# Kernel optimization log

Hardware: AMD Instinct MI355X
Metric: run time of the kernel (lower is better)

The kernel has to match this reference:

```python
import jax, jax.numpy as jnp
import numpy as np

DEPTH, C, HS, NH, WS, B = 10, 128, 512, 8, 2, 4096


def _sincos_1d(embed_dim, pos):
    omega = np.arange(embed_dim // 2, dtype=np.float64)
    omega /= embed_dim / 2.0
    omega = 1.0 / 10000 ** omega
    out = np.einsum('m,d->md', pos.reshape(-1), omega)
    return np.concatenate([np.sin(out), np.cos(out)], axis=1)


def _sincos_pos_embed(embed_dim, grid_size):
    g = np.arange(grid_size, dtype=np.float32)
    grid = np.stack(np.meshgrid(g, g), axis=0).reshape(2, -1)
    emb_h = _sincos_1d(embed_dim // 2, grid[0])
    emb_w = _sincos_1d(embed_dim // 2, grid[1])
    return np.concatenate([emb_h, emb_w], axis=1)  # (16, HS)


def _encode_board(x):
    # x: (B,128) int piece ids -> (B,12,8,8) one-hot planes (vectorized encodeBoard)
    x = x.reshape(-1, 2, 8, 8)
    pieces = jnp.arange(1, 7)
    white = (x[:, 0, None, :, :] == pieces[None, :, None, None]).astype(jnp.float32)
    black = (x[:, 1, None, :, :] == pieces[None, :, None, None]).astype(jnp.float32)
    return jnp.concatenate([white, black], axis=1)


def _conv3x3(x, w, b):
    y = jax.lax.conv_general_dilated(x, w, (1, 1), 'SAME',
                                     dimension_numbers=('NCHW', 'OIHW', 'NCHW'))
    return y + b[None, :, None, None]


def _bn(x, g, b, eps=1e-5):
    # training-mode BatchNorm2d: per-batch stats over (N,H,W)
    m = x.mean((0, 2, 3), keepdims=True)
    v = x.var((0, 2, 3), keepdims=True)
    return (x - m) * jax.lax.rsqrt(v + eps) * g[None, :, None, None] + b[None, :, None, None]


def _ln(x, eps=1e-6):
    m = x.mean(-1, keepdims=True)
    v = x.var(-1, keepdims=True)
    return (x - m) * jax.lax.rsqrt(v + eps)


def _window_partition(x, ws):
    b, c, h, w = x.shape
    x = x.reshape(b, c, h // ws, ws, w // ws, ws)
    x = x.transpose(0, 2, 4, 3, 5, 1)  # b h w p1 p2 c
    return x.reshape(b, (h // ws) * (w // ws), ws * ws * c)


def _window_reverse(win, ws, h, w):
    b, n, d = win.shape
    c = d // (ws * ws)
    x = win.reshape(b, h // ws, w // ws, ws, ws, c)
    x = x.transpose(0, 5, 1, 3, 2, 4)  # b c h p1 w p2
    return x.reshape(b, c, h, w)


def _attention(t, qkv_w, qkv_b, proj_w, proj_b):
    b, n, d = t.shape
    hd = d // NH
    qkv = (t @ qkv_w + qkv_b).reshape(b, n, 3, NH, hd)
    q, k, v = jnp.moveaxis(qkv, 2, 0)  # each (b,n,NH,hd)
    attn = jax.nn.softmax(jnp.einsum('bqhd,bkhd->bhqk', q * hd ** -0.5, k), axis=-1)
    out = jnp.einsum('bhqk,bkhd->bqhd', attn, v).reshape(b, n, d)
    return out @ proj_w + proj_b


def _block(x, pos, p):
    (rb1_w, rb1_b, g1, b1, rb2_w, rb2_b, g2, b2,
     qkv_w, qkv_b, proj_w, proj_b, f1_w, f1_b, f2_w, f2_b) = p
    h, w = x.shape[2], x.shape[3]
    z = _bn(_conv3x3(jax.nn.relu(x), rb1_w, rb1_b), g1, b1)
    z = _bn(_conv3x3(jax.nn.relu(z), rb2_w, rb2_b), g2, b2)
    x = x + z
    t = _window_partition(x, WS) + pos
    t = t + _ln(_attention(t, qkv_w, qkv_b, proj_w, proj_b))
    t = t + _ln(jax.nn.relu(t @ f1_w + f1_b) @ f2_w + f2_b)
    return _window_reverse(t, WS, h, w)


def _forward(x, pos_embed, conv1_w, conv1_b, blk, lin1_w, lin1_b, lin2_w, lin2_b):
    h = _conv3x3(_encode_board(x), conv1_w, conv1_b)

    def step(h, p):
        return _block(h, pos_embed, p), None

    h, _ = jax.lax.scan(step, h, blk)
    feat = h.transpose(0, 2, 3, 1).reshape(h.shape[0], -1)  # B (H W C)
    logits = jax.nn.relu(feat @ lin1_w + lin1_b) @ lin2_w + lin2_b
    return jax.nn.softmax(logits, axis=1)


def setup_inputs() -> dict:
    key = jax.random.key(0)
    ks = jax.random.split(key, 16)
    n = lambda k, shp: jax.random.normal(k, shp, dtype=jnp.float32) * 0.02
    inp = {}
    inp['x'] = jax.random.randint(ks[0], (B, 128), 0, 7)
    inp['pos_embed'] = jnp.asarray(_sincos_pos_embed(HS, 8 // WS), dtype=jnp.float32)[None]
    inp['conv1_w'] = n(ks[1], (C, 12, 3, 3))
    inp['conv1_b'] = jnp.zeros((C,), jnp.float32)
    inp['rb1_w'] = n(ks[2], (DEPTH, C, C, 3, 3)); inp['rb1_b'] = jnp.zeros((DEPTH, C), jnp.float32)
    inp['bn1_g'] = jnp.ones((DEPTH, C), jnp.float32); inp['bn1_b'] = jnp.zeros((DEPTH, C), jnp.float32)
    inp['rb2_w'] = n(ks[3], (DEPTH, C, C, 3, 3)); inp['rb2_b'] = jnp.zeros((DEPTH, C), jnp.float32)
    inp['bn2_g'] = jnp.ones((DEPTH, C), jnp.float32); inp['bn2_b'] = jnp.zeros((DEPTH, C), jnp.float32)
    inp['qkv_w'] = n(ks[4], (DEPTH, HS, 3 * HS)); inp['qkv_b'] = jnp.zeros((DEPTH, 3 * HS), jnp.float32)
    inp['proj_w'] = n(ks[5], (DEPTH, HS, HS)); inp['proj_b'] = jnp.zeros((DEPTH, HS), jnp.float32)
    inp['fc1_w'] = n(ks[6], (DEPTH, HS, HS)); inp['fc1_b'] = jnp.zeros((DEPTH, HS), jnp.float32)
    inp['fc2_w'] = n(ks[7], (DEPTH, HS, HS)); inp['fc2_b'] = jnp.zeros((DEPTH, HS), jnp.float32)
    inp['lin1_w'] = n(ks[8], (C * 64, 1024)); inp['lin1_b'] = jnp.zeros((1024,), jnp.float32)
    inp['lin2_w'] = n(ks[9], (1024, 640)); inp['lin2_b'] = jnp.zeros((640,), jnp.float32)
    return inp


def reference(x, pos_embed, conv1_w, conv1_b, rb1_w, rb1_b, bn1_g, bn1_b,
              rb2_w, rb2_b, bn2_g, bn2_b, qkv_w, qkv_b, proj_w, proj_b,
              fc1_w, fc1_b, fc2_w, fc2_b, lin1_w, lin1_b, lin2_w, lin2_b):
    blk = (rb1_w, rb1_b, bn1_g, bn1_b, rb2_w, rb2_b, bn2_g, bn2_b,
           qkv_w, qkv_b, proj_w, proj_b, fc1_w, fc1_b, fc2_w, fc2_b)
    return _forward(x, pos_embed, conv1_w, conv1_b, blk, lin1_w, lin1_b, lin2_w, lin2_b)
```

## Files before the change

### kernel.cpp

```cpp
#include <hip/hip_runtime.h>
#include <hip/hip_fp16.h>
#include <math.h>


#define NBATCH 4096
#define NPOSR  (NBATCH*64)
#define CH     1024
#define CHT    (CH*16)

#define OFF_ACT   0
#define OFF_BIG2  33554432
#define OFF_WT1   (OFF_BIG2 + 16777216)
#define OFF_WTA   (OFF_WT1 + 13824)
#define OFF_WTB   (OFF_WTA + 737280)
#define OFF_WTT   (OFF_WTB + 737280)
#define OFF_STATS (OFF_WTT + 786432)
#define OFF_BNP   (OFF_STATS + 256)
#define OFF_BIAS  (OFF_BNP + 256)
#define WS_NEED_FLOATS (OFF_BIAS + 1536)

#define H_QKVB 0
#define H_ATT  25165824
#define H_PRJ  0
#define H_T2H  8388608
#define H_LOG  8388608

#define T_QKV  0
#define T_PRJ  786432
#define T_F1   1048576
#define T_F2   1310720

typedef _Float16 f16x8 __attribute__((ext_vector_type(8)));
typedef _Float16 f16x4 __attribute__((ext_vector_type(4)));
typedef float f32x4 __attribute__((ext_vector_type(4)));

__device__ inline f32x4 vzero4() { f32x4 z; z[0]=0.f; z[1]=0.f; z[2]=0.f; z[3]=0.f; return z; }

__device__ inline float4 ld_half4(const __half* p) {
  float2 a = __half22float2(*(const __half2*)p);
  float2 b = __half22float2(*(const __half2*)(p + 2));
  return make_float4(a.x, a.y, b.x, b.y);
}

__device__ __forceinline__ void gll16(const void* g, void* lds) {
  __builtin_amdgcn_global_load_lds(
      (__attribute__((address_space(1))) void*)g,
      (__attribute__((address_space(3))) void*)lds,
      16, 0, 0);
}

__global__ void k_zero(float* __restrict__ s) { s[threadIdx.x] = 0.f; }

__global__ void k_sentinel(float* __restrict__ out, int n, float val) {
  for (int i = blockIdx.x*blockDim.x + threadIdx.x; i < n; i += gridDim.x*blockDim.x)
    out[i] = val;
}

__global__ void k_wprep(const float* __restrict__ src, float* __restrict__ dst, int L, int Cin) {
  int total = L * 128 * Cin * 9;
  for (int idx = blockIdx.x*blockDim.x + threadIdx.x; idx < total; idx += gridDim.x*blockDim.x) {
    int kk = idx % 9; int t2 = idx / 9;
    int ci = t2 % Cin; t2 /= Cin;
    int co = t2 % 128; int l  = t2 / 128;
    dst[((size_t)(l*9 + kk)*Cin + ci)*128 + co] = src[idx];
  }
}

__global__ void k_wprep16(const float* __restrict__ src, __half* __restrict__ dst, int L) {
  int total = L * 128 * 128 * 9;
  for (int idx = blockIdx.x*blockDim.x + threadIdx.x; idx < total; idx += gridDim.x*blockDim.x) {
    int kk = idx % 9; int t2 = idx / 9;
    int ci = t2 % 128; t2 /= 128;
    int co = t2 % 128; int l  = t2 / 128;
    dst[((size_t)(l*128 + co))*1152 + kk*128 + ci] = __float2half(src[idx]);
  }
}

__global__ void k_wt16(const float* __restrict__ W, __half* __restrict__ WT, int K, int N) {
  int total = K * N;
  for (int idx = blockIdx.x*blockDim.x + threadIdx.x; idx < total; idx += gridDim.x*blockDim.x) {
    int k = idx / N, n = idx % N;
    WT[(size_t)n*K + k] = __float2half(W[idx]);
  }
}

__global__ void k_wt16x4(const float* __restrict__ Wq, const float* __restrict__ Wp,
                         const float* __restrict__ W1, const float* __restrict__ W2,
                         const float* __restrict__ bq,
                         __half* __restrict__ wTt, float* __restrict__ biasbuf) {
  int gid0 = blockIdx.x*blockDim.x + threadIdx.x;
  if (gid0 < 1536) biasbuf[gid0] = bq[gid0] * (gid0 < 512 ? 0.125f : 1.f);
  const int TOT = 786432 + 3*262144;
  for (int idx = gid0; idx < TOT; idx += gridDim.x*blockDim.x) {
    if (idx < 786432) {
      int k = idx / 1536, n = idx % 1536;
      float v = Wq[idx] * (n < 512 ? 0.125f : 1.f);
      wTt[T_QKV + (size_t)n*512 + k] = __float2half(v);
    } else {
      int r0 = idx - 786432;
      int s = r0 / 262144, r = r0 % 262144;
      int k = r / 512, n = r % 512;
      const float* W = (s == 0) ? Wp : (s == 1) ? W1 : W2;
      wTt[T_PRJ + s*262144 + (size_t)n*512 + k] = __float2half(W[r]);
    }
  }
}

__global__ __launch_bounds__(256) void k_conv1(const int* __restrict__ xin,
    const float* __restrict__ wT1, const float* __restrict__ b1,
    float* __restrict__ out) {
  __shared__ int s_w[64], s_b[64];
  int b = blockIdx.x, t = threadIdx.x;
  if (t < 64) { s_w[t] = xin[b*128 + t]; s_b[t] = xin[b*128 + 64 + t]; }
  __syncthreads();
  int p = t >> 2, i = t & 3;
  int y = p >> 3, x = p & 7;
  float acc[32];
  #pragma unroll
  for (int j = 0; j < 32; ++j) acc[j] = b1[i*32 + j];
  #pragma unroll
  for (int kk = 0; kk < 9; ++kk) {
    int ny = y + kk/3 - 1, nx = x + kk%3 - 1;
    if (ny < 0 || ny > 7 || nx < 0 || nx > 7) continue;
    int np = ny*8 + nx;
    int wp = s_w[np], bp = s_b[np];
    if (wp >= 1 && wp <= 6) {
      const float* w = &wT1[(size_t)(kk*12 + (wp-1))*128 + i*32];
      #pragma unroll
      for (int j = 0; j < 32; ++j) acc[j] += w[j];
    }
    if (bp >= 1 && bp <= 6) {
      const float* w = &wT1[(size_t)(kk*12 + 6 + (bp-1))*128 + i*32];
      #pragma unroll
      for (int j = 0; j < 32; ++j) acc[j] += w[j];
    }
  }
  float* o = &out[((size_t)b*64 + p)*128 + i*32];
  #pragma unroll
  for (int j = 0; j < 8; ++j)
    *(float4*)&o[j*4] = make_float4(acc[j*4], acc[j*4+1], acc[j*4+2], acc[j*4+3]);
}

__device__ inline float cvt_in(float v) { return v; }
__device__ inline float cvt_in(__half v) { return __half2float(v); }

#define IMG_W 136

template<typename TIN>
__global__ __launch_bounds__(256) void k_conv_mfma(const TIN* __restrict__ in,
    const __half* __restrict__ wT , const float* __restrict__ bias,
    const float* __restrict__ bnp, int use_bn, __half* __restrict__ out,
    float* __restrict__ stats) {
  __shared__ __align__(16) _Float16 s_img[2*65*IMG_W];
  __shared__ __align__(16) _Float16 s_B[2][4096];
  __shared__ float s_sum[128], s_sq[128];
  int b2 = blockIdx.x, t = threadIdx.x;
  int w = t >> 6, lane = t & 63;

  auto issueB = [&](int win, int buf) {
    #pragma unroll
    for (int i = 0; i < 2; ++i) {
      int rbase = (w*2 + i)*16;
      const __half* g = &wT[(size_t)(rbase + (lane>>2))*1152 + win*32 + (lane&3)*8];
      gll16(g, &s_B[buf][rbase*32]);
    }
  };
  issueB(0, 0);

  for (int idx4 = t; idx4 < 4096; idx4 += 256) {
    int img = idx4 >> 11, rr = (idx4 >> 5) & 63, c4 = (idx4 & 31) * 4;
    const TIN* src = &in[((size_t)(b2*2 + img)*64 + rr)*128 + c4];
    float v0 = cvt_in(src[0]), v1 = cvt_in(src[1]), v2 = cvt_in(src[2]), v3 = cvt_in(src[3]);
    if (use_bn) {
      v0 = bnp[c4+0]*v0 + bnp[128+c4+0];
      v1 = bnp[c4+1]*v1 + bnp[128+c4+1];
      v2 = bnp[c4+2]*v2 + bnp[128+c4+2];
      v3 = bnp[c4+3]*v3 + bnp[128+c4+3];
    }
    f16x4 h;
    h[0] = (_Float16)fmaxf(v0, 0.f); h[1] = (_Float16)fmaxf(v1, 0.f);
    h[2] = (_Float16)fmaxf(v2, 0.f); h[3] = (_Float16)fmaxf(v3, 0.f);
    *(f16x4*)&s_img[(img*65 + rr)*IMG_W + c4] = h;
  }
  {
    int img = t >> 7, c = t & 127;
    s_img[(img*65 + 64)*IMG_W + c] = (_Float16)0.f;
    if (t < 128) { s_sum[t] = 0.f; s_sq[t] = 0.f; }
  }
  int wm = (w >> 1)*64, wn = (w & 1)*64;
  int fr = lane & 15, fq = lane >> 4;
  int imgo[4], yy[4], xx_[4];
  #pragma unroll
  for (int mt = 0; mt < 4; ++mt) {
    int r = wm + mt*16 + fr;
    imgo[mt] = r >> 6; int p = r & 63; yy[mt] = p >> 3; xx_[mt] = p & 7;
  }
  f32x4 acc[4][4];
  #pragma unroll
  for (int mt = 0; mt < 4; ++mt)
    #pragma unroll
    for (int nt = 0; nt < 4; ++nt) acc[mt][nt] = vzero4();
  __syncthreads();

  #pragma unroll
  for (int kk = 0; kk < 9; ++kk) {
    int dy = kk/3 - 1, dx = kk%3 - 1;
    const _Float16* abase[4];
    #pragma unroll
    for (int mt = 0; mt < 4; ++mt) {
      int ny = yy[mt] + dy, nx = xx_[mt] + dx;
      int row = ((unsigned)ny < 8u && (unsigned)nx < 8u) ? (ny*8 + nx) : 64;
      abase[mt] = &s_img[(imgo[mt]*65 + row)*IMG_W];
    }
    #pragma unroll
    for (int q = 0; q < 4; ++q) {
      int win = kk*4 + q;
      int buf = win & 1;
      if (win + 1 < 36) issueB(win + 1, buf ^ 1);
      f16x8 af[4], bf[4];
      #pragma unroll
      for (int mt = 0; mt < 4; ++mt) af[mt] = *(const f16x8*)&abase[mt][q*32 + fq*8];
      #pragma unroll
      for (int nt = 0; nt < 4; ++nt) bf[nt] = *(const f16x8*)&s_B[buf][(wn + nt*16 + fr)*32 + fq*8];
      #pragma unroll
      for (int mt = 0; mt < 4; ++mt)
        #pragma unroll
        for (int nt = 0; nt < 4; ++nt)
          acc[mt][nt] = __builtin_amdgcn_mfma_f32_16x16x32_f16(af[mt], bf[nt], acc[mt][nt], 0, 0, 0);
      __syncthreads();
    }
  }
  #pragma unroll
  for (int nt = 0; nt < 4; ++nt) {
    int col = wn + nt*16 + fr;
    float bv = bias[col];
    float s = 0.f, q = 0.f;
    #pragma unroll
    for (int mt = 0; mt < 4; ++mt) {
      int rbase = wm + mt*16 + fq*4;
      #pragma unroll
      for (int j = 0; j < 4; ++j) {
        int r = rbase + j;
        int img = r >> 6, p = r & 63;
        float v = acc[mt][nt][j] + bv;
        s += v; q += v*v;
        out[((size_t)(b2*2 + img)*64 + p)*128 + col] = __float2half(v);
      }
    }
    s += __shfl_xor(s, 16); s += __shfl_xor(s, 32);
    q += __shfl_xor(q, 16); q += __shfl_xor(q, 32);
    if (fq == 0) { atomicAdd(&s_sum[col], s); atomicAdd(&s_sq[col], q); }
  }
  __syncthreads();
  if (t < 128) {
    atomicAdd(&stats[t], s_sum[t]);
    atomicAdd(&stats[128 + t], s_sq[t]);
  }
}

__global__ void k_bnfin(float* __restrict__ stats, const float* __restrict__ g,
                        const float* __restrict__ bb, float* __restrict__ bnp) {
  int c = threadIdx.x;
  const float invN = 1.f / (float)NPOSR;
  float m = stats[c] * invN;
  float v = stats[128+c] * invN - m*m;
  float sc = g[c] * rsqrtf(v + 1e-5f);
  bnp[c] = sc;
  bnp[128+c] = bb[c] - m*sc;
  stats[c] = 0.f; stats[128+c] = 0.f;
}

__global__ __launch_bounds__(256) void k_make_t(float* __restrict__ act,
    const __half* __restrict__ z1h, const float* __restrict__ bnp,
    const float* __restrict__ pos) {
  __shared__ float s_t[8192];
  int b = blockIdx.x, t = threadIdx.x;
  for (int idx4 = t; idx4 < 2048; idx4 += 256) {
    int n = idx4 >> 7, d4 = idx4 & 127;
    int d = d4*4, c = d & 127, q = d >> 7;
    int y = ((n>>2)<<1) + (q>>1), xx = ((n&3)<<1) + (q&1);
    size_t sp = ((size_t)b*64 + y*8 + xx)*128 + c;
    float4 a  = *(const float4*)&act[sp];
    float4 z  = ld_half4(&z1h[sp]);
    float4 sc = *(const float4*)&bnp[c];
    float4 sh = *(const float4*)&bnp[128+c];
    float4 pe = *(const float4*)&pos[n*512 + d];
    float4 o;
    o.x = a.x + sc.x*z.x + sh.x + pe.x;
    o.y = a.y + sc.y*z.y + sh.y + pe.y;
    o.z = a.z + sc.z*z.z + sh.z + pe.z;
    o.w = a.w + sc.w*z.w + sh.w + pe.w;
    *(float4*)&s_t[n*512 + d] = o;
  }
  __syncthreads();
  for (int idx4 = t; idx4 < 2048; idx4 += 256)
    *(float4*)&act[(size_t)b*8192 + idx4*4] = *(float4*)&s_t[idx4*4];
}

#define QS 1544

__global__ __launch_bounds__(256) void k_attn16(const __half* __restrict__ qkvbuf,
    __half* __restrict__ attnout) {
  __shared__ __align__(16) _Float16 s_qkv[16][QS];
  __shared__ float S[8][16][17];
  int img = blockIdx.x, t = threadIdx.x;
  const __half* src = qkvbuf + (size_t)img*16*1536;
  #pragma unroll
  for (int i = 0; i < 12; ++i) {
    int lin = t + i*256;
    int row = lin / 192, c8 = lin % 192;
    *(f16x8*)&s_qkv[row][c8*8] = *(const f16x8*)&src[(size_t)row*1536 + c8*8];
  }
  __syncthreads();
  {
    int h = t >> 5, qi = (t >> 1) & 15, ko = (t & 1) * 8;
    int rot = t & 31;
    float acc[8];
    #pragma unroll
    for (int k = 0; k < 8; ++k) acc[k] = 0.f;
    const __half2* qr = (const __half2*)&s_qkv[qi][h*64];
    for (int i2 = 0; i2 < 32; ++i2) {
      int d2 = (i2 + rot) & 31;
      float2 q2 = __half22float2(qr[d2]);
      #pragma unroll
      for (int k = 0; k < 8; ++k) {
        float2 k2 = __half22float2(*(const __half2*)&s_qkv[ko + k][512 + h*64 + d2*2]);
        acc[k] += q2.x*k2.x + q2.y*k2.y;
      }
    }
    #pragma unroll
    for (int k = 0; k < 8; ++k) S[h][qi][ko + k] = acc[k];
  }
  __syncthreads();
  if (t < 128) {
    int h = t >> 4, qi = t & 15;
    float* Sr = S[h][qi];
    float mx = -1e30f;
    #pragma unroll
    for (int ki = 0; ki < 16; ++ki) mx = fmaxf(mx, Sr[ki]);
    float sm = 0.f; float e[16];
    #pragma unroll
    for (int ki = 0; ki < 16; ++ki) { e[ki] = expf(Sr[ki] - mx); sm += e[ki]; }
    float inv = 1.f / sm;
    #pragma unroll
    for (int ki = 0; ki < 16; ++ki) Sr[ki] = e[ki]*inv;
  }
  __syncthreads();
  {
    int qi = t >> 4, rem = t & 15;
    int h = rem >> 1, dhb = (rem & 1) * 32;
    int rot = (t >> 2) & 15;
    float P[16];
    #pragma unroll
    for (int k = 0; k < 16; ++k) P[k] = S[h][qi][(k + rot) & 15];
    __half* orow = attnout + ((size_t)img*16 + qi)*512 + h*64 + dhb;
    #pragma unroll
    for (int j = 0; j < 16; ++j) {
      int dh = dhb + 2*j;
      float a0 = 0.f, a1 = 0.f;
      #pragma unroll
      for (int kk2 = 0; kk2 < 16; ++kk2) {
        int ki = (kk2 + rot) & 15;
        float2 v2 = __half22float2(*(const __half2*)&s_qkv[ki][1024 + h*64 + dh]);
        a0 += P[kk2]*v2.x; a1 += P[kk2]*v2.y;
      }
      *(__half2*)&orow[2*j] = __floats2half2_rn(a0, a1);
    }
  }
}

template<int MTI, int A16, int B16, int RELU, int OUT16>
__global__ __launch_bounds__(256) void k_mgemm(const void* __restrict__ Ap,
    const void* __restrict__ Bp, const float* __restrict__ bias,
    void* __restrict__ Cp, int M, int N, int K) {
  constexpr int BM = MTI*32;
  __shared__ __align__(16) _Float16 sA[2][BM*32];
  __shared__ __align__(16) _Float16 sB[2][128*32];
  int t = threadIdx.x;
  int bm = blockIdx.x * BM, bn = blockIdx.y * 128;
  int w = t >> 6, lane = t & 63;
  int wm = (w >> 1) * (MTI*16), wn = (w & 1) * 64;
  int fr = lane & 15, fq = lane >> 4;

  auto stageA = [&](int k0, int buf) {
    if (A16) {
      const __half* A = (const __half*)Ap;
      constexpr int NI = MTI/2;
      #pragma unroll
      for (int i = 0; i < NI; ++i) {
        int rbase = (w*NI + i)*16;
        gll16(&A[(size_t)(bm + rbase + (lane>>2))*K + k0 + (lane&3)*8],
              &sA[buf][rbase*32]);
      }
    } else {
      const float* A = (const float*)Ap;
      if (MTI == 4) {
        int srow = t >> 1, skh = (t & 1) * 16;
        const float4* src = (const float4*)&A[(size_t)(bm + srow)*K + k0 + skh];
        float4 v0 = src[0], v1 = src[1], v2 = src[2], v3 = src[3];
        f16x8 h0, h1;
        h0[0]=(_Float16)v0.x; h0[1]=(_Float16)v0.y; h0[2]=(_Float16)v0.z; h0[3]=(_Float16)v0.w;
        h0[4]=(_Float16)v1.x; h0[5]=(_Float16)v1.y; h0[6]=(_Float16)v1.z; h0[7]=(_Float16)v1.w;
        h1[0]=(_Float16)v2.x; h1[1]=(_Float16)v2.y; h1[2]=(_Float16)v2.z; h1[3]=(_Float16)v2.w;
        h1[4]=(_Float16)v3.x; h1[5]=(_Float16)v3.y; h1[6]=(_Float16)v3.z; h1[7]=(_Float16)v3.w;
        *(f16x8*)&sA[buf][srow*32 + skh]     = h0;
        *(f16x8*)&sA[buf][srow*32 + skh + 8] = h1;
      } else {
        int srow = t >> 2, g8 = (t & 3) * 8;
        const float4* src = (const float4*)&A[(size_t)(bm + srow)*K + k0 + g8];
        float4 v0 = src[0], v1 = src[1];
        f16x8 h0;
        h0[0]=(_Float16)v0.x; h0[1]=(_Float16)v0.y; h0[2]=(_Float16)v0.z; h0[3]=(_Float16)v0.w;
        h0[4]=(_Float16)v1.x; h0[5]=(_Float16)v1.y; h0[6]=(_Float16)v1.z; h0[7]=(_Float16)v1.w;
        *(f16x8*)&sA[buf][srow*32 + g8] = h0;
      }
    }
  };
  auto stageB = [&](int k0, int buf) {
    if (B16) {
      const __half* BT = (const __half*)Bp;
      #pragma unroll
      for (int i = 0; i < 2; ++i) {
        int rbase = (w*2 + i)*16;
        gll16(&BT[(size_t)(bn + rbase + (lane>>2))*K + k0 + (lane&3)*8],
              &sB[buf][rbase*32]);
      }
    } else {
      const float* B = (const float*)Bp;
      int kr = t >> 3, n0 = (t & 7) * 16;
      #pragma unroll
      for (int g = 0; g < 4; ++g) {
        float4 v = *(const float4*)&B[(size_t)(k0 + kr)*N + bn + n0 + g*4];
        sB[buf][(n0+g*4+0)*32 + kr] = (_Float16)v.x;
        sB[buf][(n0+g*4+1)*32 + kr] = (_Float16)v.y;
        sB[buf][(n0+g*4+2)*32 + kr] = (_Float16)v.z;
        sB[buf][(n0+g*4+3)*32 + kr] = (_Float16)v.w;
      }
    }
  };

  f32x4 acc[MTI][4];
  #pragma unroll
  for (int mt = 0; mt < MTI; ++mt)
    #pragma unroll
    for (int nt = 0; nt < 4; ++nt) acc[mt][nt] = vzero4();

  stageA(0, 0); stageB(0, 0);
  __syncthreads();
  int KW = K >> 5;
  for (int kw = 0; kw < KW; ++kw) {
    int buf = kw & 1;
    if (kw + 1 < KW) { stageA((kw+1)*32, buf ^ 1); stageB((kw+1)*32, buf ^ 1); }
    f16x8 af[MTI], bf[4];
    #pragma unroll
    for (int mt = 0; mt < MTI; ++mt) af[mt] = *(const f16x8*)&sA[buf][(wm + mt*16 + fr)*32 + fq*8];
    #pragma unroll
    for (int nt = 0; nt < 4; ++nt) bf[nt] = *(const f16x8*)&sB[buf][(wn + nt*16 + fr)*32 + fq*8];
    #pragma unroll
    for (int mt = 0; mt < MTI; ++mt)
      #pragma unroll
      for (int nt = 0; nt < 4; ++nt)
        acc[mt][nt] = __builtin_amdgcn_mfma_f32_16x16x32_f16(af[mt], bf[nt], acc[mt][nt], 0, 0, 0);
    __syncthreads();
  }
  #pragma unroll
  for (int mt = 0; mt < MTI; ++mt)
    #pragma unroll
    for (int nt = 0; nt < 4; ++nt) {
      int col = bn + wn + nt*16 + fr;
      float bv = bias[col];
      #pragma unroll
      for (int j = 0; j < 4; ++j) {
        int row = bm + wm + mt*16 + fq*4 + j;
        float v = acc[mt][nt][j] + bv;
        if (RELU) v = fmaxf(v, 0.f);
        if (OUT16) ((__half*)Cp)[(size_t)row*N + col] = __float2half(v);
        else       ((float*)Cp)[(size_t)row*N + col] = v;
      }
    }
}

__global__ __launch_bounds__(256) void k_lnres(const __half* __restrict__ pout,
    float* __restrict__ tact, __half* __restrict__ t2h) {
  int t = threadIdx.x;
  int tok = blockIdx.x*4 + (t >> 6);
  int lane = t & 63;
  f16x8 hv = *(const f16x8*)&pout[(size_t)tok*512 + lane*8];
  float v[8]; float s1 = 0.f, s2 = 0.f;
  #pragma unroll
  for (int j = 0; j < 8; ++j) { v[j] = (float)hv[j]; s1 += v[j]; s2 += v[j]*v[j]; }
  #pragma unroll
  for (int m = 32; m >= 1; m >>= 1) { s1 += __shfl_xor(s1, m); s2 += __shfl_xor(s2, m); }
  float mean = s1 * (1.f/512.f);
  float var  = s2 * (1.f/512.f) - mean*mean;
  float rs = rsqrtf(var + 1e-6f);
  float* ar = &tact[(size_t)tok*512 + lane*8];
  f16x8 o16;
  #pragma unroll
  for (int j = 0; j < 8; ++j) {
    float t2 = ar[j] + (v[j] - mean)*rs;
    ar[j] = t2;
    o16[j] = (_Float16)t2;
  }
  *(f16x8*)&t2h[(size_t)tok*512 + lane*8] = o16;
}

__global__ __launch_bounds__(256) void k_lnres2(const __half* __restrict__ fout,
    float* __restrict__ actimg) {
  __shared__ float s_t2[8192];
  int bimg = blockIdx.x, t = threadIdx.x;
  int lane = t & 63;
  for (int tg = 0; tg < 4; ++tg) {
    int n = tg*4 + (t >> 6);
    size_t row = (size_t)bimg*16 + n;
    f16x8 hv = *(const f16x8*)&fout[row*512 + lane*8];
    float v[8]; float s1 = 0.f, s2 = 0.f;
    #pragma unroll
    for (int j = 0; j < 8; ++j) { v[j] = (float)hv[j]; s1 += v[j]; s2 += v[j]*v[j]; }
    #pragma unroll
    for (int m = 32; m >= 1; m >>= 1) { s1 += __shfl_xor(s1, m); s2 += __shfl_xor(s2, m); }
    float mean = s1 * (1.f/512.f);
    float var  = s2 * (1.f/512.f) - mean*mean;
    float rs = rsqrtf(var + 1e-6f);
    const float* ar = &actimg[row*512 + lane*8];
    #pragma unroll
    for (int j = 0; j < 8; ++j) s_t2[n*512 + lane*8 + j] = ar[j] + (v[j] - mean)*rs;
  }
  __syncthreads();
  for (int idx = t; idx < 2048; idx += 256) {
    int p = idx >> 5, c = (idx & 31)*4;
    int y = p >> 3, x = p & 7;
    int n = (y >> 1)*4 + (x >> 1);
    int d = ((y & 1)*2 + (x & 1))*128 + c;
    *(float4*)&actimg[(size_t)bimg*8192 + p*128 + c] = *(float4*)&s_t2[n*512 + d];
  }
}

__global__ __launch_bounds__(256) void k_softmax(const float* __restrict__ logits, float* __restrict__ out) {
  int b = blockIdx.x, t = threadIdx.x;
  __shared__ float red[256];
  float m = -1e30f;
  for (int j = t; j < 640; j += 256) m = fmaxf(m, logits[(size_t)b*640 + j]);
  red[t] = m; __syncthreads();
  for (int s = 128; s > 0; s >>= 1) { if (t < s) red[t] = fmaxf(red[t], red[t+s]); __syncthreads(); }
  m = red[0]; __syncthreads();
  float sum = 0.f;
  for (int j = t; j < 640; j += 256) sum += expf(logits[(size_t)b*640 + j] - m);
  red[t] = sum; __syncthreads();
  for (int s = 128; s > 0; s >>= 1) { if (t < s) red[t] += red[t+s]; __syncthreads(); }
  float inv = 1.f / red[0];
  for (int j = t; j < 640; j += 256) out[(size_t)b*640 + j] = expf(logits[(size_t)b*640 + j] - m) * inv;
}

extern "C" void kernel_launch(void* const* d_in, const int* in_sizes, int n_in,
                              void* d_out, int out_size, void* d_ws, size_t ws_size,
                              hipStream_t stream) {
  (void)in_sizes; (void)n_in;
  float* out = (float*)d_out;
  if (ws_size < (size_t)WS_NEED_FLOATS * 4) {
    k_sentinel<<<2048, 256, 0, stream>>>(out, out_size, (float)(ws_size >> 20));
    return;
  }

  const int*   x       = (const int*)d_in[0];
  const float* pos     = (const float*)d_in[1];
  const float* conv1_w = (const float*)d_in[2];
  const float* conv1_b = (const float*)d_in[3];
  const float* rb1_w   = (const float*)d_in[4];
  const float* rb1_b   = (const float*)d_in[5];
  const float* bn1_g   = (const float*)d_in[6];
  const float* bn1_b   = (const float*)d_in[7];
  const float* rb2_w   = (const float*)d_in[8];
  const float* rb2_b   = (const float*)d_in[9];
  const float* bn2_g   = (const float*)d_in[10];
  const float* bn2_b   = (const float*)d_in[11];
  const float* qkv_w   = (const float*)d_in[12];
  const float* qkv_b   = (const float*)d_in[13];
  const float* proj_w  = (const float*)d_in[14];
  const float* proj_b  = (const float*)d_in[15];
  const float* fc1_w   = (const float*)d_in[16];
  const float* fc1_b   = (const float*)d_in[17];
  const float* fc2_w   = (const float*)d_in[18];
  const float* fc2_b   = (const float*)d_in[19];
  const float* lin1_w  = (const float*)d_in[20];
  const float* lin1_b  = (const float*)d_in[21];
  const float* lin2_w  = (const float*)d_in[22];
  const float* lin2_b  = (const float*)d_in[23];

  float*  ws    = (float*)d_ws;
  float*  act   = ws + OFF_ACT;
  __half* big2h = (__half*)(ws + OFF_BIG2);
  float*  wT1   = ws + OFF_WT1;
  __half* wTa16 = (__half*)(ws + OFF_WTA);
  __half* wTb16 = (__half*)(ws + OFF_WTB);
  __half* wTt   = (__half*)(ws + OFF_WTT);
  float*  stats = ws + OFF_STATS;
  float*  bnp   = ws + OFF_BNP;
  float*  biasbuf = ws + OFF_BIAS;

  __half* z1h     = big2h;
  __half* qkvbuf  = big2h + H_QKVB;
  __half* attnout = big2h + H_ATT;
  __half* projout = big2h + H_PRJ;
  __half* t2h     = big2h + H_T2H;
  __half* h1      = attnout;
  __half* fc2out  = projout;
  __half* qkvT    = wTt + T_QKV;
  __half* projT   = wTt + T_PRJ;
  __half* fc1T    = wTt + T_F1;
  __half* fc2T    = wTt + T_F2;
  __half* L1h     = big2h;
  float*  logits  = (float*)(big2h + H_LOG);
  __half* lin2T   = wTt;

  k_zero<<<1, 256, 0, stream>>>(stats);
  k_wprep<<<64, 256, 0, stream>>>(conv1_w, wT1, 1, 12);
  k_wprep16<<<2048, 256, 0, stream>>>(rb1_w, wTa16, 10);
  k_wprep16<<<2048, 256, 0, stream>>>(rb2_w, wTb16, 10);
  k_conv1<<<NBATCH, 256, 0, stream>>>(x, wT1, conv1_b, act);

  for (int l = 0; l < 10; ++l) {
    k_conv_mfma<float><<<NBATCH/2, 256, 0, stream>>>(act, wTa16 + (size_t)l*147456,
        rb1_b + l*128, (const float*)nullptr, 0, z1h, stats);
    k_bnfin<<<1, 128, 0, stream>>>(stats, bn1_g + l*128, bn1_b + l*128, bnp);
    k_conv_mfma<__half><<<NBATCH/2, 256, 0, stream>>>(z1h, wTb16 + (size_t)l*147456,
        rb2_b + l*128, bnp, 1, z1h, stats);
    k_bnfin<<<1, 128, 0, stream>>>(stats, bn2_g + l*128, bn2_b + l*128, bnp);
    k_make_t<<<NBATCH, 256, 0, stream>>>(act, z1h, bnp, pos);

    k_wt16x4<<<2048, 256, 0, stream>>>(qkv_w + (size_t)l*786432,
        proj_w + (size_t)l*262144, fc1_w + (size_t)l*262144, fc2_w + (size_t)l*262144,
        qkv_b + l*1536, wTt, biasbuf);

    for (int ch = 0; ch < NBATCH/CH; ++ch) {
      float* tchunk = act + (size_t)ch*CH*8192;
      k_mgemm<4,0,1,0,1><<<dim3(CHT/128, 12), 256, 0, stream>>>(tchunk, qkvT,
          biasbuf, qkvbuf, CHT, 1536, 512);
      k_attn16<<<CH, 256, 0, stream>>>(qkvbuf, attnout);
      k_mgemm<4,1,1,0,1><<<dim3(CHT/128, 4), 256, 0, stream>>>(attnout, projT,
          proj_b + l*512, projout, CHT, 512, 512);
      k_lnres<<<CHT/4, 256, 0, stream>>>(projout, tchunk, t2h);
      k_mgemm<4,1,1,1,1><<<dim3(CHT/128, 4), 256, 0, stream>>>(t2h, fc1T,
          fc1_b + l*512, h1, CHT, 512, 512);
      k_mgemm<4,1,1,0,1><<<dim3(CHT/128, 4), 256, 0, stream>>>(h1, fc2T,
          fc2_b + l*512, fc2out, CHT, 512, 512);
      k_lnres2<<<CH, 256, 0, stream>>>(fc2out, tchunk);
    }
  }
  k_mgemm<2,0,0,1,1><<<dim3(4096/64, 8), 256, 0, stream>>>(act, lin1_w, lin1_b, L1h,
      4096, 1024, 8192);
  k_wt16<<<512, 256, 0, stream>>>(lin2_w, lin2T, 1024, 640);
  k_mgemm<2,1,1,0,0><<<dim3(4096/64, 5), 256, 0, stream>>>(L1h, lin2T, lin2_b, logits,
      4096, 640, 1024);
  k_softmax<<<NBATCH, 256, 0, stream>>>(logits, out);
}
```

Measured before the change: 10.16 ms.

## Fuse proj/fc2 GEMMs with LayerNorm residual epilogue and window-reverse scatter

Replaces the proj and fc2 GEMMs plus their separate LayerNorm-residual kernels with one GEMM kernel whose block covers a full 512-wide row (32 rows x 512 cols). Row statistics are reduced across waves in shared memory, and the epilogue applies the residual LN. For fc2 the epilogue also writes straight back in image layout. This removes the fp16 intermediate round trip and two launches per chunk. In exchange it uses smaller M tiles with a full B panel (32KB per buffer) in LDS, and its epilogue global accesses are scattered and less coalesced.

```diff
diff --git a/kernel.cpp b/kernel.cpp
--- a/kernel.cpp
+++ b/kernel.cpp
@@ -21,7 +21,6 @@
 
 #define H_QKVB 0
 #define H_ATT  25165824
-#define H_PRJ  0
 #define H_T2H  8388608
 #define H_LOG  8388608
 
@@ -480,59 +479,149 @@
     }
 }
 
-__global__ __launch_bounds__(256) void k_lnres(const __half* __restrict__ pout,
+template<int FC2>
+__global__ __launch_bounds__(256) void k_gemm_ln(const __half* __restrict__ Ap,
+    const __half* __restrict__ BT, const float* __restrict__ bias,
     float* __restrict__ tact, __half* __restrict__ t2h) {
+  const int K = 512;
+  __shared__ __align__(16) _Float16 sA[2][32*32];
+  __shared__ __align__(16) _Float16 sB[2][512*32];
+  __shared__ float s_p1[4][32], s_p2[4][32];
+  __shared__ float s_mean[32], s_rs[32];
   int t = threadIdx.x;
-  int tok = blockIdx.x*4 + (t >> 6);
-  int lane = t & 63;
-  f16x8 hv = *(const f16x8*)&pout[(size_t)tok*512 + lane*8];
-  float v[8]; float s1 = 0.f, s2 = 0.f;
-  #pragma unroll
-  for (int j = 0; j < 8; ++j) { v[j] = (float)hv[j]; s1 += v[j]; s2 += v[j]*v[j]; }
-  #pragma unroll
-  for (int m = 32; m >= 1; m >>= 1) { s1 += __shfl_xor(s1, m); s2 += __shfl_xor(s2, m); }
-  float mean = s1 * (1.f/512.f);
-  float var  = s2 * (1.f/512.f) - mean*mean;
-  float rs = rsqrtf(var + 1e-6f);
-  float* ar = &tact[(size_t)tok*512 + lane*8];
-  f16x8 o16;
-  #pragma unroll
-  for (int j = 0; j < 8; ++j) {
-    float t2 = ar[j] + (v[j] - mean)*rs;
-    ar[j] = t2;
-    o16[j] = (_Float16)t2;
-  }
-  *(f16x8*)&t2h[(size_t)tok*512 + lane*8] = o16;
-}
-
-__global__ __launch_bounds__(256) void k_lnres2(const __half* __restrict__ fout,
-    float* __restrict__ actimg) {
-  __shared__ float s_t2[8192];
-  int bimg = blockIdx.x, t = threadIdx.x;
-  int lane = t & 63;
-  for (int tg = 0; tg < 4; ++tg) {
-    int n = tg*4 + (t >> 6);
-    size_t row = (size_t)bimg*16 + n;
-    f16x8 hv = *(const f16x8*)&fout[row*512 + lane*8];
-    float v[8]; float s1 = 0.f, s2 = 0.f;
-    #pragma unroll
-    for (int j = 0; j < 8; ++j) { v[j] = (float)hv[j]; s1 += v[j]; s2 += v[j]*v[j]; }
-    #pragma unroll
-    for (int m = 32; m >= 1; m >>= 1) { s1 += __shfl_xor(s1, m); s2 += __shfl_xor(s2, m); }
+  int bm = blockIdx.x * 32;
+  int w = t >> 6, lane = t & 63;
+  int wn = w * 128;
+  int fr = lane & 15, fq = lane >> 4;
+
+  auto stageA = [&](int k0, int buf) {
+    if (w < 2) {
+      int rbase = w*16;
+      gll16(&Ap[(size_t)(bm + rbase + (lane>>2))*K + k0 + (lane&3)*8], &sA[buf][rbase*32]);
+    }
+  };
+  auto stageB = [&](int k0, int buf) {
+    #pragma unroll
+    for (int i = 0; i < 8; ++i) {
+      int rbase = (w*8 + i)*16;
+      gll16(&BT[(size_t)(rbase + (lane>>2))*K + k0 + (lane&3)*8], &sB[buf][rbase*32]);
+    }
+  };
+
+  f32x4 acc[2][8];
+  #pragma unroll
+  for (int mt = 0; mt < 2; ++mt)
+    #pragma unroll
+    for (int nt = 0; nt < 8; ++nt) acc[mt][nt] = vzero4();
+
+  stageA(0, 0); stageB(0, 0);
+  __syncthreads();
+  for (int kw = 0; kw < 16; ++kw) {
+    int buf = kw & 1;
+    if (kw + 1 < 16) { stageA((kw+1)*32, buf ^ 1); stageB((kw+1)*32, buf ^ 1); }
+    f16x8 af[2], bf[8];
+    #pragma unroll
+    for (int mt = 0; mt < 2; ++mt) af[mt] = *(const f16x8*)&sA[buf][(mt*16 + fr)*32 + fq*8];
+    #pragma unroll
+    for (int nt = 0; nt < 8; ++nt) bf[nt] = *(const f16x8*)&sB[buf][(wn + nt*16 + fr)*32 + fq*8];
+    #pragma unroll
+    for (int mt = 0; mt < 2; ++mt)
+      #pragma unroll
+      for (int nt = 0; nt < 8; ++nt)
+        acc[mt][nt] = __builtin_amdgcn_mfma_f32_16x16x32_f16(af[mt], bf[nt], acc[mt][nt], 0, 0, 0);
+    __syncthreads();
+  }
+  float rs1[2][4], rs2[2][4];
+  #pragma unroll
+  for (int mt = 0; mt < 2; ++mt)
+    #pragma unroll
+    for (int j = 0; j < 4; ++j) { rs1[mt][j] = 0.f; rs2[mt][j] = 0.f; }
+  #pragma unroll
+  for (int mt = 0; mt < 2; ++mt)
+    #pragma unroll
+    for (int nt = 0; nt < 8; ++nt) {
+      float bv = bias[wn + nt*16 + fr];
+      #pragma unroll
+      for (int j = 0; j < 4; ++j) {
+        float v = acc[mt][nt][j] + bv;
+        acc[mt][nt][j] = v;
+        rs1[mt][j] += v; rs2[mt][j] += v*v;
+      }
+    }
+  #pragma unroll
+  for (int m = 1; m <= 8; m <<= 1) {
+    #pragma unroll
+    for (int mt = 0; mt < 2; ++mt)
+      #pragma unroll
+      for (int j = 0; j < 4; ++j) {
+        rs1[mt][j] += __shfl_xor(rs1[mt][j], m);
+        rs2[mt][j] += __shfl_xor(rs2[mt][j], m);
+      }
+  }
+  if (fr == 0) {
+    #pragma unroll
+    for (int mt = 0; mt < 2; ++mt)
+      #pragma unroll
+      for (int j = 0; j < 4; ++j) {
+        int r = mt*16 + fq*4 + j;
+        s_p1[w][r] = rs1[mt][j]; s_p2[w][r] = rs2[mt][j];
+      }
+  }
+  __syncthreads();
+  if (t < 32) {
+    float s1 = s_p1[0][t] + s_p1[1][t] + s_p1[2][t] + s_p1[3][t];
+    float s2 = s_p2[0][t] + s_p2[1][t] + s_p2[2][t] + s_p2[3][t];
     float mean = s1 * (1.f/512.f);
     float var  = s2 * (1.f/512.f) - mean*mean;
-    float rs = rsqrtf(var + 1e-6f);
-    const float* ar = &actimg[row*512 + lane*8];
-    #pragma unroll
-    for (int j = 0; j < 8; ++j) s_t2[n*512 + lane*8 + j] = ar[j] + (v[j] - mean)*rs;
-  }
-  __syncthreads();
-  for (int idx = t; idx < 2048; idx += 256) {
-    int p = idx >> 5, c = (idx & 31)*4;
-    int y = p >> 3, x = p & 7;
-    int n = (y >> 1)*4 + (x >> 1);
-    int d = ((y & 1)*2 + (x & 1))*128 + c;
-    *(float4*)&actimg[(size_t)bimg*8192 + p*128 + c] = *(float4*)&s_t2[n*512 + d];
+    s_mean[t] = mean; s_rs[t] = rsqrtf(var + 1e-6f);
+  }
+  __syncthreads();
+  if (!FC2) {
+    #pragma unroll
+    for (int mt = 0; mt < 2; ++mt)
+      #pragma unroll
+      for (int j = 0; j < 4; ++j) {
+        int r = mt*16 + fq*4 + j;
+        float mean = s_mean[r], rsv = s_rs[r];
+        size_t tok = (size_t)(bm + r);
+        #pragma unroll
+        for (int nt = 0; nt < 8; ++nt) {
+          int col = wn + nt*16 + fr;
+          float t2 = tact[tok*512 + col] + (acc[mt][nt][j] - mean)*rsv;
+          tact[tok*512 + col] = t2;
+          t2h[tok*512 + col] = __float2half(t2);
+        }
+      }
+  } else {
+    #pragma unroll
+    for (int mt = 0; mt < 2; ++mt)
+      #pragma unroll
+      for (int j = 0; j < 4; ++j) {
+        int r = mt*16 + fq*4 + j;
+        float mean = s_mean[r], rsv = s_rs[r];
+        size_t tok = (size_t)(bm + r);
+        #pragma unroll
+        for (int nt = 0; nt < 8; ++nt) {
+          int col = wn + nt*16 + fr;
+          acc[mt][nt][j] = tact[tok*512 + col] + (acc[mt][nt][j] - mean)*rsv;
+        }
+      }
+    __syncthreads();
+    #pragma unroll
+    for (int mt = 0; mt < 2; ++mt)
+      #pragma unroll
+      for (int j = 0; j < 4; ++j) {
+        int r = mt*16 + fq*4 + j;
+        int tok = bm + r;
+        int img = tok >> 4, n = tok & 15;
+        #pragma unroll
+        for (int nt = 0; nt < 8; ++nt) {
+          int d = wn + nt*16 + fr;
+          int q = d >> 7, c = d & 127;
+          int y = ((n>>2)<<1) + (q>>1), xx = ((n&3)<<1) + (q&1);
+          tact[((size_t)img*64 + y*8 + xx)*128 + c] = acc[mt][nt][j];
+        }
+      }
   }
 }
 
@@ -601,10 +690,8 @@
   __half* z1h     = big2h;
   __half* qkvbuf  = big2h + H_QKVB;
   __half* attnout = big2h + H_ATT;
-  __half* projout = big2h + H_PRJ;
   __half* t2h     = big2h + H_T2H;
   __half* h1      = attnout;
-  __half* fc2out  = projout;
   __half* qkvT    = wTt + T_QKV;
   __half* projT   = wTt + T_PRJ;
   __half* fc1T    = wTt + T_F1;
@@ -637,14 +724,12 @@
       k_mgemm<4,0,1,0,1><<<dim3(CHT/128, 12), 256, 0, stream>>>(tchunk, qkvT,
           biasbuf, qkvbuf, CHT, 1536, 512);
       k_attn16<<<CH, 256, 0, stream>>>(qkvbuf, attnout);
-      k_mgemm<4,1,1,0,1><<<dim3(CHT/128, 4), 256, 0, stream>>>(attnout, projT,
-          proj_b + l*512, projout, CHT, 512, 512);
-      k_lnres<<<CHT/4, 256, 0, stream>>>(projout, tchunk, t2h);
+      k_gemm_ln<0><<<CHT/32, 256, 0, stream>>>(attnout, projT, proj_b + l*512,
+          tchunk, t2h);
       k_mgemm<4,1,1,1,1><<<dim3(CHT/128, 4), 256, 0, stream>>>(t2h, fc1T,
           fc1_b + l*512, h1, CHT, 512, 512);
-      k_mgemm<4,1,1,0,1><<<dim3(CHT/128, 4), 256, 0, stream>>>(h1, fc2T,
-          fc2_b + l*512, fc2out, CHT, 512, 512);
-      k_lnres2<<<CH, 256, 0, stream>>>(fc2out, tchunk);
+      k_gemm_ln<1><<<CHT/32, 256, 0, stream>>>(h1, fc2T, fc2_b + l*512,
+          tchunk, t2h);
     }
   }
   k_mgemm<2,0,0,1,1><<<dim3(4096/64, 8), 256, 0, stream>>>(act, lin1_w, lin1_b, L1h,
```

Result: slower. 10.70 ms (+5.3%).
